# Kernel optimization log

Hardware: AMD Instinct MI355X
Metric: run time of the kernel (lower is better)

Reference implementation:

```python
import jax, jax.numpy as jnp
import numpy as np

B, T, D, H = 2, 2048, 1024, 16
HS = D // H
EPS = 1e-5


def setup_inputs() -> dict:
    key = jax.random.key(0)
    ks = jax.random.split(key, 16)
    s = lambda *shape: 0.02
    inp = {
        "x": jax.random.normal(ks[0], (B, T, D), jnp.float32),
        # per-head Q/K/V weights stacked over heads: [H, D, HS]
        "Wq": jax.random.normal(ks[1], (H, D, HS), jnp.float32) * 0.02,
        "bq": jnp.zeros((H, HS), jnp.float32),
        "Wk": jax.random.normal(ks[2], (H, D, HS), jnp.float32) * 0.02,
        "bk": jnp.zeros((H, HS), jnp.float32),
        "Wv": jax.random.normal(ks[3], (H, D, HS), jnp.float32) * 0.02,
        "bv": jnp.zeros((H, HS), jnp.float32),
        "Wp": jax.random.normal(ks[4], (D, D), jnp.float32) * 0.02,
        "bp": jnp.zeros((D,), jnp.float32),
        "W1": jax.random.normal(ks[5], (D, 4 * D), jnp.float32) * 0.02,
        "b1": jnp.zeros((4 * D,), jnp.float32),
        "W2": jax.random.normal(ks[6], (4 * D, D), jnp.float32) * 0.02,
        "b2": jnp.zeros((D,), jnp.float32),
        "g1": jnp.ones((D,), jnp.float32),
        "be1": jnp.zeros((D,), jnp.float32),
        "g2": jnp.ones((D,), jnp.float32),
        "be2": jnp.zeros((D,), jnp.float32),
    }
    return inp


def layernorm(x, g, b):
    mu = jnp.mean(x, axis=-1, keepdims=True)
    var = jnp.mean(jnp.square(x - mu), axis=-1, keepdims=True)
    return (x - mu) * jax.lax.rsqrt(var + EPS) * g + b


def reference(x, Wq, bq, Wk, bk, Wv, bv, Wp, bp, W1, b1, W2, b2, g1, be1, g2, be2):
    # NOTE: this block applies LN then residual-adds the *normalized* x,
    # exactly as in the original (x = ln1(x); x = x + mha(x)).
    h = layernorm(x, g1, be1)
    # multi-head attention, all heads batched via stacked weights
    q = jnp.einsum('btd,hdk->bhtk', h, Wq) + bq[None, :, None, :]
    k = jnp.einsum('btd,hdk->bhtk', h, Wk) + bk[None, :, None, :]
    v = jnp.einsum('btd,hdk->bhtk', h, Wv) + bv[None, :, None, :]
    att = jnp.einsum('bhtk,bhsk->bhts', q, k) * (HS ** -0.5)  # [B,H,T,T]
    att = jax.nn.softmax(att, axis=-1)
    o = jnp.einsum('bhts,bhsk->bhtk', att, v)  # [B,H,T,HS]
    # concat heads in order along last dim -> [B,T,D]
    o = jnp.transpose(o, (0, 2, 1, 3)).reshape(B, T, D)
    o = o @ Wp + bp
    h = h + o
    h2 = layernorm(h, g2, be2)
    ff = jax.nn.gelu(h2 @ W1 + b1, approximate=False) @ W2 + b2
    return h2 + ff
```

## Files before the change

kernel.cpp:

```cpp
#include <hip/hip_runtime.h>
#include <cstdint>
#include <cstddef>

#define B_  2
#define T_  2048
#define D_  1024
#define H_  16
#define HS_ 64
#define MTOT (B_*T_)

typedef unsigned short u16;
typedef __attribute__((ext_vector_type(8))) __bf16 bf16x8;
typedef __attribute__((ext_vector_type(4))) float f32x4;

__device__ __forceinline__ u16 f2bf(float f) {
  unsigned int u = __builtin_bit_cast(unsigned int, f);
  u += 0x7fffu + ((u >> 16) & 1u);
  return (u16)(u >> 16);
}

__device__ __forceinline__ unsigned cvtpk(float lo, float hi) {
  unsigned r;
  asm("v_cvt_pk_bf16_f32 %0, %1, %2" : "=v"(r) : "v"(lo), "v"(hi));
  return r;
}

__device__ __forceinline__ void gload16(const u16* g, u16* l) {
  __builtin_amdgcn_global_load_lds((const __attribute__((address_space(1))) void*)g,
                                   (__attribute__((address_space(3))) void*)l, 16, 0, 0);
}

__global__ __launch_bounds__(256) void transpose_f2b(const float* __restrict__ in,
                                                     u16* __restrict__ out, int R, int C) {
  __shared__ float tile[32][33];
  int c0 = blockIdx.x * 32, r0 = blockIdx.y * 32;
  size_t zoff = (size_t)blockIdx.z * R * C;
  const float* src = in + zoff;
  u16* dst = out + zoff;
  int tx = threadIdx.x & 31, ty = threadIdx.x >> 5;
#pragma unroll
  for (int k = 0; k < 4; ++k)
    tile[ty + k*8][tx] = src[(size_t)(r0 + ty + k*8) * C + c0 + tx];
  __syncthreads();
#pragma unroll
  for (int k = 0; k < 4; ++k)
    dst[(size_t)(c0 + ty + k*8) * R + r0 + tx] = f2bf(tile[tx][ty + k*8]);
}

__global__ __launch_bounds__(256) void transpose_v(const u16* __restrict__ in,
                                                   u16* __restrict__ out) {
  __shared__ u16 tile[32][33];
  int z = blockIdx.z;
  int b = z >> 4, h = z & 15;
  int t0 = blockIdx.x * 32, f0 = blockIdx.y * 32;
  int tx = threadIdx.x & 31, ty = threadIdx.x >> 5;
#pragma unroll
  for (int k = 0; k < 4; ++k)
    tile[ty + k*8][tx] = in[((size_t)b*T_ + t0 + ty + k*8) * D_ + h*HS_ + f0 + tx];
  __syncthreads();
#pragma unroll
  for (int k = 0; k < 4; ++k)
    out[((size_t)z*HS_ + f0 + ty + k*8) * T_ + t0 + tx] = tile[tx][ty + k*8];
}

__global__ __launch_bounds__(256) void ln_kernel(const float* __restrict__ x,
                                                 const float* __restrict__ gg,
                                                 const float* __restrict__ be,
                                                 float* __restrict__ hf,
                                                 u16* __restrict__ hb) {
  int row = blockIdx.x;
  int t = threadIdx.x;
  const float* xr = x + (size_t)row * D_;
  float4 xv = *(const float4*)&xr[t * 4];
  float s  = xv.x + xv.y + xv.z + xv.w;
  float ss = xv.x*xv.x + xv.y*xv.y + xv.z*xv.z + xv.w*xv.w;
#pragma unroll
  for (int m = 1; m < 64; m <<= 1) { s += __shfl_xor(s, m); ss += __shfl_xor(ss, m); }
  __shared__ float red[8];
  int lane = t & 63, wv = t >> 6;
  if (lane == 0) { red[wv] = s; red[4 + wv] = ss; }
  __syncthreads();
  s  = red[0] + red[1] + red[2] + red[3];
  ss = red[4] + red[5] + red[6] + red[7];
  float mu  = s * (1.0f / D_);
  float var = ss * (1.0f / D_) - mu * mu;
  float rs  = rsqrtf(var + 1e-5f);
  float4 gv = *(const float4*)&gg[t * 4];
  float4 bv = *(const float4*)&be[t * 4];
  float4 hv;
  hv.x = (xv.x - mu) * rs * gv.x + bv.x;
  hv.y = (xv.y - mu) * rs * gv.y + bv.y;
  hv.z = (xv.z - mu) * rs * gv.z + bv.z;
  hv.w = (xv.w - mu) * rs * gv.w + bv.w;
  *(float4*)&hf[(size_t)row * D_ + t * 4] = hv;
  uint2 pk;
  pk.x = (unsigned)f2bf(hv.x) | ((unsigned)f2bf(hv.y) << 16);
  pk.y = (unsigned)f2bf(hv.z) | ((unsigned)f2bf(hv.w) << 16);
  *(uint2*)&hb[(size_t)row * D_ + t * 4] = pk;
}

template<int EPI>
__global__ __launch_bounds__(512, 2) void gemm256(
    const u16* __restrict__ A, const u16* __restrict__ Bt,
    const float* __restrict__ bias0, const float* __restrict__ bias1,
    const float* __restrict__ bias2,
    u16* __restrict__ o0, u16* __restrict__ o1, u16* __restrict__ o2,
    int M, int N, int K) {
  __shared__ __align__(16) u16 As[2][256 * 64];
  __shared__ __align__(16) u16 Bs[2][256 * 64];
  const int tid = threadIdx.x;
  const int lane = tid & 63, w = tid >> 6;
  const int m0 = blockIdx.y * 256, n0 = blockIdx.x * 256;
  const int rA = lane & 15, g = lane >> 4;
  const int wm = (w >> 2) * 128, wn = (w & 3) * 64;
  const int sxa = rA & 7;

  f32x4 acc[8][4] = {};

  auto stage = [&](int t, int bufi) {
#pragma unroll
    for (int i = 0; i < 4; ++i) {
      int c = i * 512 + tid;
      int row = c >> 3;
      int ss = (c & 7) ^ (row & 7);
      gload16(A + (size_t)(m0 + row) * K + t * 64 + ss * 8,
              &As[bufi][0] + (size_t)(i * 512 + w * 64) * 8);
    }
#pragma unroll
    for (int i = 0; i < 4; ++i) {
      int c = i * 512 + tid;
      int row = c >> 3;
      int ss = (c & 7) ^ (row & 7);
      gload16(Bt + (size_t)(n0 + row) * K + t * 64 + ss * 8,
              &Bs[bufi][0] + (size_t)(i * 512 + w * 64) * 8);
    }
  };

  stage(0, 0);

  const int nk = K >> 6;
  for (int t = 0; t < nk; ++t) {
    __syncthreads();
    const int buf = t & 1;
    if (t + 1 < nk) stage(t + 1, buf ^ 1);

    bf16x8 bfr[4][2];
#pragma unroll
    for (int j = 0; j < 4; ++j) {
      int br = wn + j * 16 + rA;
#pragma unroll
      for (int kk = 0; kk < 2; ++kk)
        bfr[j][kk] = *(const bf16x8*)&Bs[buf][br * 64 + (((kk * 4 + g) ^ sxa) << 3)];
    }
#pragma unroll
    for (int i = 0; i < 8; ++i) {
      int ar = wm + i * 16 + rA;
      bf16x8 a0 = *(const bf16x8*)&As[buf][ar * 64 + ((g ^ sxa) << 3)];
      bf16x8 a1 = *(const bf16x8*)&As[buf][ar * 64 + (((4 + g) ^ sxa) << 3)];
#pragma unroll
      for (int j = 0; j < 4; ++j) {
        acc[i][j] = __builtin_amdgcn_mfma_f32_16x16x32_bf16(a0, bfr[j][0], acc[i][j], 0, 0, 0);
        acc[i][j] = __builtin_amdgcn_mfma_f32_16x16x32_bf16(a1, bfr[j][1], acc[i][j], 0, 0, 0);
      }
    }
  }

#pragma unroll
  for (int i = 0; i < 8; ++i) {
#pragma unroll
    for (int j = 0; j < 4; ++j) {
#pragma unroll
      for (int r = 0; r < 4; ++r) {
        int row = m0 + wm + i * 16 + g * 4 + r;
        int col = n0 + wn + j * 16 + rA;
        float v = acc[i][j][r];
        if constexpr (EPI == 0) {
          int sel = col >> 10, nn = col & 1023;
          const float* bp = sel == 0 ? bias0 : (sel == 1 ? bias1 : bias2);
          u16* op = sel == 0 ? o0 : (sel == 1 ? o1 : o2);
          op[(size_t)row * 1024 + nn] = f2bf(v + bp[nn]);
        } else {
          v += bias0[col];
          float z = 0.7978845608f * (v + 0.044715f * v * v * v);
          z = fminf(z, 18.0f);
          float e = __builtin_amdgcn_exp2f(z * 2.8853900817779268f);
          v = v * e / (e + 1.0f);
          o0[(size_t)row * N + col] = f2bf(v);
        }
      }
    }
  }
}

template<int EPI>
__global__ __launch_bounds__(256) void gemm_bt(
    const u16* __restrict__ A, const u16* __restrict__ Bt,
    const float* __restrict__ bias0, const float* __restrict__ res,
    float* __restrict__ outf, float* __restrict__ p1,
    int M, int N, int K, int kLen) {
  __shared__ __align__(16) u16 As[3][128 * 32];
  __shared__ __align__(16) u16 Bs[3][128 * 32];
  const int tid = threadIdx.x;
  const int lane = tid & 63, wv = tid >> 6;
  const int m0 = blockIdx.y * 128, n0 = blockIdx.x * 128;
  const int kOff = blockIdx.z * kLen;
  const int rA = lane & 15, g = lane >> 4;
  const int wm = (wv >> 1) * 64, wn = (wv & 1) * 64;
  const int sx = (rA >> 1) & 3;

  f32x4 acc[4][4] = {};

  auto stage = [&](int tt, int bufi) {
#pragma unroll
    for (int p = 0; p < 2; ++p) {
      int c = (p * 4 + wv) * 64 + lane;
      int row = c >> 2;
      int s = (c & 3) ^ ((row >> 1) & 3);
      gload16(A  + (size_t)(m0 + row) * K + kOff + tt * 32 + s * 8,
              &As[bufi][0] + (size_t)(p * 4 + wv) * 512);
      gload16(Bt + (size_t)(n0 + row) * K + kOff + tt * 32 + s * 8,
              &Bs[bufi][0] + (size_t)(p * 4 + wv) * 512);
    }
  };

  const int nk = kLen >> 5;
  stage(0, 0);
  stage(1, 1);

  int cur = 0, nxt = 2;
  for (int t = 0; t < nk; ++t) {
    if (t + 1 < nk) asm volatile("s_waitcnt vmcnt(4)" ::: "memory");
    else            asm volatile("s_waitcnt vmcnt(0)" ::: "memory");
    __builtin_amdgcn_s_barrier();
    __builtin_amdgcn_sched_barrier(0);
    if (t + 2 < nk) stage(t + 2, nxt);

    bf16x8 a[4], b[4];
#pragma unroll
    for (int i = 0; i < 4; ++i)
      a[i] = *(const bf16x8*)&As[cur][(wm + i * 16 + rA) * 32 + ((g ^ sx) << 3)];
#pragma unroll
    for (int i = 0; i < 4; ++i)
      b[i] = *(const bf16x8*)&Bs[cur][(wn + i * 16 + rA) * 32 + ((g ^ sx) << 3)];
#pragma unroll
    for (int i = 0; i < 4; ++i)
#pragma unroll
      for (int j = 0; j < 4; ++j)
        acc[i][j] = __builtin_amdgcn_mfma_f32_16x16x32_bf16(a[i], b[j], acc[i][j], 0, 0, 0);

    cur = (cur == 2) ? 0 : cur + 1;
    nxt = (nxt == 2) ? 0 : nxt + 1;
  }

#pragma unroll
  for (int i = 0; i < 4; ++i) {
#pragma unroll
    for (int j = 0; j < 4; ++j) {
#pragma unroll
      for (int r = 0; r < 4; ++r) {
        int row = m0 + wm + i * 16 + g * 4 + r;
        int col = n0 + wn + j * 16 + rA;
        float v = acc[i][j][r];
        if constexpr (EPI == 2) {
          v += bias0[col] + res[(size_t)row * N + col];
          outf[(size_t)row * N + col] = v;
        } else {
          float* dst = blockIdx.z ? p1 : outf;
          dst[(size_t)row * N + col] = v;
        }
      }
    }
  }
}

__global__ __launch_bounds__(256) void reduce_ff2(const float* __restrict__ p0,
                                                  const float* __restrict__ p1,
                                                  const float* __restrict__ bias,
                                                  const float* __restrict__ res,
                                                  float* __restrict__ out) {
  int i = (blockIdx.x * 256 + threadIdx.x) * 4;
  float4 a = *(const float4*)&p0[i];
  float4 b = *(const float4*)&p1[i];
  float4 r = *(const float4*)&res[i];
  float4 bb = *(const float4*)&bias[i & 1023];
  float4 o;
  o.x = a.x + b.x + r.x + bb.x;
  o.y = a.y + b.y + r.y + bb.y;
  o.z = a.z + b.z + r.z + bb.z;
  o.w = a.w + b.w + r.w + bb.w;
  *(float4*)&out[i] = o;
}

__global__ __launch_bounds__(256) void attn_kernel(const u16* __restrict__ qg,
                                                   const u16* __restrict__ kg,
                                                   const u16* __restrict__ vtg,
                                                   u16* __restrict__ og) {
  const int wg = blockIdx.x;
  const int qt = wg & 31;
  const int h  = (wg >> 5) & 15;
  const int b  = wg >> 9;
  const int tid = threadIdx.x, lane = tid & 63, wv = tid >> 6;
  const int q0 = qt * 64 + wv * 16;
  const int rA = lane & 15, g = lane >> 4;
  const int rx = rA & 7;

  __shared__ __align__(16) u16 Ks[2][64 * 64];
  __shared__ __align__(16) u16 Vs[2][64 * 64];
  __shared__ __align__(16) u16 Ps[4][16 * 64];

  const size_t qoff = ((size_t)b * T_ + q0 + rA) * D_ + h * HS_ + g * 8;
  const bf16x8 aq0 = *(const bf16x8*)&qg[qoff];
  const bf16x8 aq1 = *(const bf16x8*)&qg[qoff + 32];

  const u16* kbase = kg + (size_t)b * T_ * D_ + h * HS_;
  const u16* vbase = vtg + ((size_t)b * H_ + h) * HS_ * T_;

  const float cfold = 0.18033688011112042f;
  float mrun = -1e30f, lrun = 0.0f;
  f32x4 oacc[4] = {};

  auto stage = [&](int t, int buf) {
#pragma unroll
    for (int p = 0; p < 2; ++p) {
      int chunk = p * 256 + wv * 64 + lane;
      int row = chunk >> 3, s = chunk & 7;
      int ss = s ^ (row & 7);
      gload16(kbase + ((size_t)t * 64 + row) * D_ + ss * 8,
              &Ks[buf][0] + (size_t)(p * 256 + wv * 64) * 8);
      gload16(vbase + (size_t)row * T_ + t * 64 + ss * 8,
              &Vs[buf][0] + (size_t)(p * 256 + wv * 64) * 8);
    }
  };

  stage(0, 0);

  const int NT = T_ / 64;
  for (int t = 0; t < NT; ++t) {
    __syncthreads();
    const int buf = t & 1;
    if (t + 1 < NT) stage(t + 1, buf ^ 1);

    const u16* kb = &Ks[buf][0];
    f32x4 sc[4];
    __builtin_amdgcn_s_setprio(1);
#pragma unroll
    for (int st = 0; st < 4; ++st) {
      bf16x8 k0 = *(const bf16x8*)&kb[(st * 16 + rA) * 64 + ((g ^ rx) << 3)];
      bf16x8 k1 = *(const bf16x8*)&kb[(st * 16 + rA) * 64 + (((4 + g) ^ rx) << 3)];
      f32x4 z = {};
      z = __builtin_amdgcn_mfma_f32_16x16x32_bf16(k0, aq0, z, 0, 0, 0);
      z = __builtin_amdgcn_mfma_f32_16x16x32_bf16(k1, aq1, z, 0, 0, 0);
      sc[st] = z;
    }
    __builtin_amdgcn_s_setprio(0);

    float a0 = fmaxf(fmaxf(sc[0][0], sc[0][1]), fmaxf(sc[0][2], sc[0][3]));
    float a1 = fmaxf(fmaxf(sc[1][0], sc[1][1]), fmaxf(sc[1][2], sc[1][3]));
    float a2 = fmaxf(fmaxf(sc[2][0], sc[2][1]), fmaxf(sc[2][2], sc[2][3]));
    float a3 = fmaxf(fmaxf(sc[3][0], sc[3][1]), fmaxf(sc[3][2], sc[3][3]));
    float mx = fmaxf(fmaxf(a0, a1), fmaxf(a2, a3));
    mx = fmaxf(mx, __shfl_xor(mx, 16));
    mx = fmaxf(mx, __shfl_xor(mx, 32));
    float tm = mx * cfold;

    if (__any(tm > mrun + 8.0f)) {
      float mnew = fmaxf(mrun, tm);
      float sca = __builtin_amdgcn_exp2f(mrun - mnew);
      mrun = mnew;
      lrun *= sca;
#pragma unroll
      for (int f = 0; f < 4; ++f) oacc[f] *= sca;
    }

    float p[16];
#pragma unroll
    for (int st = 0; st < 4; ++st)
#pragma unroll
      for (int r = 0; r < 4; ++r)
        p[st * 4 + r] = __builtin_amdgcn_exp2f(__builtin_fmaf(sc[st][r], cfold, -mrun));

    float sum = (((p[0] + p[1]) + (p[2] + p[3])) + ((p[4] + p[5]) + (p[6] + p[7])))
              + (((p[8] + p[9]) + (p[10] + p[11])) + ((p[12] + p[13]) + (p[14] + p[15])));
    sum += __shfl_xor(sum, 16);
    sum += __shfl_xor(sum, 32);
    lrun += sum;

    char* psb = (char*)&Ps[wv][0];
#pragma unroll
    for (int st = 0; st < 4; ++st) {
      uint2 w;
      w.x = cvtpk(p[st * 4 + 0], p[st * 4 + 1]);
      w.y = cvtpk(p[st * 4 + 2], p[st * 4 + 3]);
      int slot = st * 2 + (g >> 1);
      *(uint2*)&psb[rA * 128 + (((slot ^ rx)) << 4) + ((g & 1) << 3)] = w;
    }
    bf16x8 pf0 = *(const bf16x8*)&psb[rA * 128 + ((g ^ rx) << 4)];
    bf16x8 pf1 = *(const bf16x8*)&psb[rA * 128 + (((4 + g) ^ rx) << 4)];

    const u16* vbl = &Vs[buf][0];
    __builtin_amdgcn_s_setprio(1);
#pragma unroll
    for (int f = 0; f < 4; ++f) {
      bf16x8 v0 = *(const bf16x8*)&vbl[(f * 16 + rA) * 64 + ((g ^ rx) << 3)];
      bf16x8 v1 = *(const bf16x8*)&vbl[(f * 16 + rA) * 64 + (((4 + g) ^ rx) << 3)];
      oacc[f] = __builtin_amdgcn_mfma_f32_16x16x32_bf16(v0, pf0, oacc[f], 0, 0, 0);
      oacc[f] = __builtin_amdgcn_mfma_f32_16x16x32_bf16(v1, pf1, oacc[f], 0, 0, 0);
    }
    __builtin_amdgcn_s_setprio(0);
  }

  float linv = 1.0f / lrun;
#pragma unroll
  for (int f = 0; f < 4; ++f) {
    uint2 w;
    w.x = cvtpk(oacc[f][0] * linv, oacc[f][1] * linv);
    w.y = cvtpk(oacc[f][2] * linv, oacc[f][3] * linv);
    *(uint2*)&og[((size_t)b * T_ + q0 + rA) * D_ + h * HS_ + f * 16 + g * 4] = w;
  }
}

extern "C" void kernel_launch(void* const* d_in, const int* in_sizes, int n_in,
                              void* d_out, int out_size, void* d_ws, size_t ws_size,
                              hipStream_t stream) {
  const float* x   = (const float*)d_in[0];
  const float* Wq  = (const float*)d_in[1];
  const float* bq  = (const float*)d_in[2];
  const float* Wk  = (const float*)d_in[3];
  const float* bk  = (const float*)d_in[4];
  const float* Wv  = (const float*)d_in[5];
  const float* bv  = (const float*)d_in[6];
  const float* Wp  = (const float*)d_in[7];
  const float* bp  = (const float*)d_in[8];
  const float* W1  = (const float*)d_in[9];
  const float* b1  = (const float*)d_in[10];
  const float* W2  = (const float*)d_in[11];
  const float* b2  = (const float*)d_in[12];
  const float* g1  = (const float*)d_in[13];
  const float* be1 = (const float*)d_in[14];
  const float* g2  = (const float*)d_in[15];
  const float* be2 = (const float*)d_in[16];
  float* out = (float*)d_out;

  char* w = (char*)d_ws;
  auto alloc = [&](size_t bytes) { char* p = w; w += (bytes + 255) & ~(size_t)255; return p; };
  const size_t MD = (size_t)MTOT * D_;

  float* h_f    = (float*)alloc(MD * 4);
  u16*   h_b    = (u16*)  alloc(MD * 2);
  u16*   wqkv_t = (u16*)  alloc(3 * (size_t)D_ * D_ * 2);
  u16*   wp_t   = (u16*)  alloc((size_t)D_ * D_ * 2);
  u16*   w1_t   = (u16*)  alloc((size_t)D_ * 4 * D_ * 2);
  u16*   w2_t   = (u16*)  alloc((size_t)D_ * 4 * D_ * 2);
  u16*   q_b    = (u16*)  alloc(MD * 2);
  u16*   k_b    = (u16*)  alloc(MD * 2);
  u16*   v_b    = (u16*)  alloc(MD * 2);
  u16*   vt_b   = (u16*)  alloc(MD * 2);
  u16*   o_b    = (u16*)  alloc(MD * 2);
  float* hat_f  = (float*)alloc(MD * 4);
  u16*   ff1_b  = q_b;
  float* h2_f   = h_f;
  u16*   h2_b   = h_b;
  float* pf0    = hat_f;
  float* pf1    = (float*)h_b;

  dim3 blk(256);

  transpose_f2b<<<dim3(2, 32, 16), blk, 0, stream>>>(Wq, wqkv_t, 1024, 64);
  transpose_f2b<<<dim3(2, 32, 16), blk, 0, stream>>>(Wk, wqkv_t + (size_t)D_ * D_, 1024, 64);
  transpose_f2b<<<dim3(2, 32, 16), blk, 0, stream>>>(Wv, wqkv_t + 2 * (size_t)D_ * D_, 1024, 64);
  transpose_f2b<<<dim3(32, 32, 1), blk, 0, stream>>>(Wp, wp_t, 1024, 1024);
  transpose_f2b<<<dim3(128, 32, 1), blk, 0, stream>>>(W1, w1_t, 1024, 4096);
  transpose_f2b<<<dim3(32, 128, 1), blk, 0, stream>>>(W2, w2_t, 4096, 1024);

  ln_kernel<<<dim3(MTOT), blk, 0, stream>>>(x, g1, be1, h_f, h_b);

  gemm256<0><<<dim3(12, 16), dim3(512), 0, stream>>>(h_b, wqkv_t, bq, bk, bv,
      q_b, k_b, v_b, MTOT, 3072, 1024);

  transpose_v<<<dim3(64, 2, 32), blk, 0, stream>>>(v_b, vt_b);

  attn_kernel<<<dim3(B_ * H_ * (T_ / 64)), blk, 0, stream>>>(q_b, k_b, vt_b, o_b);

  gemm_bt<2><<<dim3(8, 32, 1), blk, 0, stream>>>(o_b, wp_t, bp, h_f, hat_f,
      nullptr, MTOT, 1024, 1024, 1024);

  ln_kernel<<<dim3(MTOT), blk, 0, stream>>>(hat_f, g2, be2, h2_f, h2_b);

  gemm256<1><<<dim3(16, 16), dim3(512), 0, stream>>>(h2_b, w1_t, b1, nullptr, nullptr,
      ff1_b, nullptr, nullptr, MTOT, 4096, 1024);

  gemm_bt<3><<<dim3(8, 32, 2), blk, 0, stream>>>(ff1_b, w2_t, nullptr, nullptr,
      pf0, pf1, MTOT, 1024, 4096, 2048);

  reduce_ff2<<<dim3(MTOT), blk, 0, stream>>>(pf0, pf1, b2, h2_f, out);
}
```

Before: 282.3 us.

## Deepen GEMM pipeline to four K-32 LDS stages with explicit vmcnt waits

Rewrites the 256x256 bf16 GEMM main loop from a double-buffered K=64 pipeline into a four-slot ring of K=32 tiles. It prefetches three stages ahead and waits with explicit s_waitcnt vmcnt counts plus a raw s_barrier, instead of a __syncthreads per step. It also adds an XCD-style workgroup index swizzle, so neighbouring tiles are scheduled to the same group and L2 reuse improves, and it changes the LDS XOR swizzle to fit the 32-wide rows. The aim is to hide global-load latency better. In exchange there are twice as many barriers per K, and correctness relies on the hand-counted vmcnt values.

```diff
diff --git a/kernel.cpp b/kernel.cpp
--- a/kernel.cpp
+++ b/kernel.cpp
@@ -106,62 +106,64 @@
     const float* __restrict__ bias2,
     u16* __restrict__ o0, u16* __restrict__ o1, u16* __restrict__ o2,
     int M, int N, int K) {
-  __shared__ __align__(16) u16 As[2][256 * 64];
-  __shared__ __align__(16) u16 Bs[2][256 * 64];
+  __shared__ __align__(16) u16 As[4][256 * 32];
+  __shared__ __align__(16) u16 Bs[4][256 * 32];
   const int tid = threadIdx.x;
   const int lane = tid & 63, w = tid >> 6;
-  const int m0 = blockIdx.y * 256, n0 = blockIdx.x * 256;
+  const int nwg = gridDim.x * gridDim.y;
+  const int flat = blockIdx.y * gridDim.x + blockIdx.x;
+  const int swz = (flat & 7) * (nwg >> 3) + (flat >> 3);
+  const int m0 = (swz / gridDim.x) * 256, n0 = (swz % gridDim.x) * 256;
   const int rA = lane & 15, g = lane >> 4;
   const int wm = (w >> 2) * 128, wn = (w & 3) * 64;
-  const int sxa = rA & 7;
+  const int sx = (rA >> 1) & 3;
 
   f32x4 acc[8][4] = {};
 
-  auto stage = [&](int t, int bufi) {
-#pragma unroll
-    for (int i = 0; i < 4; ++i) {
+  auto stage = [&](int tt, int bufi) {
+#pragma unroll
+    for (int i = 0; i < 2; ++i) {
       int c = i * 512 + tid;
-      int row = c >> 3;
-      int ss = (c & 7) ^ (row & 7);
-      gload16(A + (size_t)(m0 + row) * K + t * 64 + ss * 8,
-              &As[bufi][0] + (size_t)(i * 512 + w * 64) * 8);
-    }
-#pragma unroll
-    for (int i = 0; i < 4; ++i) {
+      int row = c >> 2;
+      int s = (c & 3) ^ ((row >> 1) & 3);
+      gload16(A + (size_t)(m0 + row) * K + tt * 32 + s * 8,
+              &As[bufi][0] + (size_t)c * 8);
+    }
+#pragma unroll
+    for (int i = 0; i < 2; ++i) {
       int c = i * 512 + tid;
-      int row = c >> 3;
-      int ss = (c & 7) ^ (row & 7);
-      gload16(Bt + (size_t)(n0 + row) * K + t * 64 + ss * 8,
-              &Bs[bufi][0] + (size_t)(i * 512 + w * 64) * 8);
+      int row = c >> 2;
+      int s = (c & 3) ^ ((row >> 1) & 3);
+      gload16(Bt + (size_t)(n0 + row) * K + tt * 32 + s * 8,
+              &Bs[bufi][0] + (size_t)c * 8);
     }
   };
 
+  const int nk = K >> 5;
   stage(0, 0);
-
-  const int nk = K >> 6;
+  stage(1, 1);
+  stage(2, 2);
+
   for (int t = 0; t < nk; ++t) {
-    __syncthreads();
-    const int buf = t & 1;
-    if (t + 1 < nk) stage(t + 1, buf ^ 1);
-
-    bf16x8 bfr[4][2];
-#pragma unroll
-    for (int j = 0; j < 4; ++j) {
-      int br = wn + j * 16 + rA;
-#pragma unroll
-      for (int kk = 0; kk < 2; ++kk)
-        bfr[j][kk] = *(const bf16x8*)&Bs[buf][br * 64 + (((kk * 4 + g) ^ sxa) << 3)];
-    }
+    const int rem = nk - 1 - t;
+    if      (rem >= 2) asm volatile("s_waitcnt vmcnt(8)" ::: "memory");
+    else if (rem == 1) asm volatile("s_waitcnt vmcnt(4)" ::: "memory");
+    else               asm volatile("s_waitcnt vmcnt(0)" ::: "memory");
+    __builtin_amdgcn_s_barrier();
+    __builtin_amdgcn_sched_barrier(0);
+    if (t + 3 < nk) stage(t + 3, (t + 3) & 3);
+    const int buf = t & 3;
+
+    bf16x8 b[4];
+#pragma unroll
+    for (int j = 0; j < 4; ++j)
+      b[j] = *(const bf16x8*)&Bs[buf][(wn + j * 16 + rA) * 32 + ((g ^ sx) << 3)];
 #pragma unroll
     for (int i = 0; i < 8; ++i) {
-      int ar = wm + i * 16 + rA;
-      bf16x8 a0 = *(const bf16x8*)&As[buf][ar * 64 + ((g ^ sxa) << 3)];
-      bf16x8 a1 = *(const bf16x8*)&As[buf][ar * 64 + (((4 + g) ^ sxa) << 3)];
-#pragma unroll
-      for (int j = 0; j < 4; ++j) {
-        acc[i][j] = __builtin_amdgcn_mfma_f32_16x16x32_bf16(a0, bfr[j][0], acc[i][j], 0, 0, 0);
-        acc[i][j] = __builtin_amdgcn_mfma_f32_16x16x32_bf16(a1, bfr[j][1], acc[i][j], 0, 0, 0);
-      }
+      bf16x8 a = *(const bf16x8*)&As[buf][(wm + i * 16 + rA) * 32 + ((g ^ sx) << 3)];
+#pragma unroll
+      for (int j = 0; j < 4; ++j)
+        acc[i][j] = __builtin_amdgcn_mfma_f32_16x16x32_bf16(a, b[j], acc[i][j], 0, 0, 0);
     }
   }
 
```

Measured after the change: 299.8 us. +6.2%, slower.
